# Performance work log

Hardware: AMD Instinct MI355X
Metric: run time of the kernel (lower is better)

## Reference

```python
import jax, jax.numpy as jnp
import numpy as np

BEV_H = 128; BEV_W = 128; HEADS = 8; POINTS = 4; NUM_LAYERS = 6
PC = (-51.2, -51.2, -5.0, 51.2, 51.2, 3.0)
EPS = 1e-5


def _layernorm(x, g, b):
    m = x.mean(-1, keepdims=True)
    v = x.var(-1, keepdims=True)
    return (x - m) * jax.lax.rsqrt(v + 1e-5) * g + b


def _bilinear(feat, loc):
    # feat: (H, W, D); loc: (..., 2) normalized xy in [0, 1]; zero padding outside.
    H, W = feat.shape[0], feat.shape[1]
    ix = loc[..., 0] * W - 0.5
    iy = loc[..., 1] * H - 0.5
    x0 = jnp.floor(ix); y0 = jnp.floor(iy)
    fx = ix - x0; fy = iy - y0
    out = 0.0
    for dx in (0, 1):
        for dy in (0, 1):
            xi = x0 + dx; yi = y0 + dy
            w = (fx if dx else 1.0 - fx) * (fy if dy else 1.0 - fy)
            m = (xi >= 0) & (xi < W) & (yi >= 0) & (yi < H)
            xi_c = jnp.clip(xi, 0, W - 1).astype(jnp.int32)
            yi_c = jnp.clip(yi, 0, H - 1).astype(jnp.int32)
            out = out + (w * m)[..., None] * feat[yi_c, xi_c]
    return out


def _deform_grid(q, value, H, W, ref, ow, ob, aw, ab):
    # Deformable attention over a (H, W) grid of values; q: (Nq, C), value: (H*W, C).
    Nq, C = q.shape
    hd = C // HEADS
    v = value.reshape(H, W, HEADS, hd).transpose(2, 0, 1, 3)            # (h, H, W, hd)
    off = (q @ ow + ob).reshape(Nq, HEADS, POINTS, 2)
    loc = ref[:, None, None, :] + off / jnp.array([W, H], q.dtype)      # (Nq, h, P, 2)
    attn = jax.nn.softmax((q @ aw + ab).reshape(Nq, HEADS, POINTS), axis=-1)
    sampled = jax.vmap(_bilinear)(v, loc.transpose(1, 0, 2, 3))         # (h, Nq, P, hd)
    return jnp.einsum('hnpd,nhp->nhd', sampled, attn).reshape(Nq, C)


def _sca(q, feats, ref_cam, valid, ow, ob, aw, ab):
    # Spatial cross-attention: feats (Ncam, h, Hf, Wf, hd), ref_cam (Ncam, Nq, P, 2),
    # valid (Ncam, Nq, P) float mask of in-frustum projections.
    Nq, C = q.shape
    Hf, Wf = feats.shape[2], feats.shape[3]
    off = (q @ ow + ob).reshape(Nq, HEADS, POINTS, 2)
    loc = ref_cam[:, None] + (off / jnp.array([Wf, Hf], q.dtype)).transpose(1, 0, 2, 3)[None]
    # loc: (Ncam, h, Nq, P, 2)
    attn = jax.nn.softmax((q @ aw + ab).reshape(Nq, HEADS, POINTS), axis=-1)
    sampled = jax.vmap(jax.vmap(_bilinear))(feats, loc)                 # (Ncam, h, Nq, P, hd)
    num = jnp.einsum('chnpd,nhp,cnp->nhd', sampled, attn, valid)
    cnt = jnp.maximum(valid.sum((0, 2)), 1.0)                           # (Nq,)
    return (num / cnt[:, None, None]).reshape(Nq, C)


def _forward(image_feats, camera_intrinsics, camera_extrinsics, prev_bev, bev_embed,
             tsa_vw, tsa_vb, tsa_ow, tsa_ob, tsa_aw, tsa_ab, tsa_pw, tsa_pb,
             sca_vw, sca_vb, sca_ow, sca_ob, sca_aw, sca_ab, sca_pw, sca_pb,
             ffn_w1, ffn_b1, ffn_w2, ffn_b2,
             ln1_g, ln1_b, ln2_g, ln2_b, ln3_g, ln3_b):
    Ncam, C, Hf, Wf = image_feats.shape
    hd = C // HEADS
    Nq = BEV_H * BEV_W
    dt = image_feats.dtype
    feats_flat = image_feats.transpose(0, 2, 3, 1).reshape(Ncam * Hf * Wf, C)

    # 2D reference points for temporal self-attention (each query's own cell).
    xs = (jnp.arange(BEV_W, dtype=dt) + 0.5) / BEV_W
    ys = (jnp.arange(BEV_H, dtype=dt) + 0.5) / BEV_H
    gx, gy = jnp.meshgrid(xs, ys)                                       # (H, W) each
    ref2d = jnp.stack([gx.reshape(-1), gy.reshape(-1)], -1)             # (Nq, 2)

    # 3D pillar reference points projected into each camera.
    xm = PC[0] + gx.reshape(-1) * (PC[3] - PC[0])
    ym = PC[1] + gy.reshape(-1) * (PC[4] - PC[1])
    zm = PC[2] + (jnp.arange(POINTS, dtype=dt) + 0.5) / POINTS * (PC[5] - PC[2])
    ref3d = jnp.stack([
        jnp.broadcast_to(xm[:, None], (Nq, POINTS)),
        jnp.broadcast_to(ym[:, None], (Nq, POINTS)),
        jnp.broadcast_to(zm[None, :], (Nq, POINTS)),
        jnp.ones((Nq, POINTS), dt)], -1)                                # (Nq, P, 4)
    ego2cam = jnp.linalg.inv(camera_extrinsics[0])                      # (Ncam, 4, 4)
    pcam = jnp.einsum('cij,npj->cnpi', ego2cam, ref3d)[..., :3]
    img = jnp.einsum('cij,cnpj->cnpi', camera_intrinsics[0], pcam)
    z = img[..., 2]
    un = img[..., 0] / (jnp.maximum(z, EPS) * Wf)
    vn = img[..., 1] / (jnp.maximum(z, EPS) * Hf)
    valid = ((z > EPS) & (un >= 0) & (un <= 1) & (vn >= 0) & (vn <= 1)).astype(dt)
    ref_cam = jnp.stack([un, vn], -1)                                   # (Ncam, Nq, P, 2)

    q = bev_embed                                                       # (Nq, C)
    prev = prev_bev[:, 0, :]                                            # (Nq, C), B = 1
    for l in range(NUM_LAYERS):
        # Temporal self-attention: deformable sampling from prev BEV + current BEV.
        v_prev = prev @ tsa_vw[l] + tsa_vb[l]
        v_cur = q @ tsa_vw[l] + tsa_vb[l]
        a = 0.5 * (_deform_grid(q, v_prev, BEV_H, BEV_W, ref2d, tsa_ow[l], tsa_ob[l], tsa_aw[l], tsa_ab[l])
                   + _deform_grid(q, v_cur, BEV_H, BEV_W, ref2d, tsa_ow[l], tsa_ob[l], tsa_aw[l], tsa_ab[l]))
        q = _layernorm(q + a @ tsa_pw[l] + tsa_pb[l], ln1_g[l], ln1_b[l])
        # Spatial cross-attention over multi-camera image features.
        v_img = (feats_flat @ sca_vw[l] + sca_vb[l]).reshape(Ncam, Hf, Wf, HEADS, hd).transpose(0, 3, 1, 2, 4)
        a = _sca(q, v_img, ref_cam, valid, sca_ow[l], sca_ob[l], sca_aw[l], sca_ab[l])
        q = _layernorm(q + a @ sca_pw[l] + sca_pb[l], ln2_g[l], ln2_b[l])
        # FFN
        a = jax.nn.relu(q @ ffn_w1[l] + ffn_b1[l]) @ ffn_w2[l] + ffn_b2[l]
        q = _layernorm(q + a, ln3_g[l], ln3_b[l])
    return q.T.reshape(1, C, BEV_H, BEV_W)


def setup_inputs() -> dict:
    key = jax.random.key(0)
    ks = iter(jax.random.split(key, 80))
    def nrm(shape, s=0.02):
        return jax.random.normal(next(ks), shape, jnp.float32) * s
    C, L, Ncam, Hf, Wf = 256, NUM_LAYERS, 6, 58, 100
    Nq = BEV_H * BEV_W
    HP, HP2 = HEADS * POINTS, HEADS * POINTS * 2
    # Structured nuScenes-like cameras: 6 yaws at 60 deg, intrinsics at feature-map scale.
    extr = np.zeros((1, Ncam, 4, 4), np.float32)
    for c in range(Ncam):
        t = c * np.pi / 3.0
        f = np.array([np.cos(t), np.sin(t), 0.0])
        xc = np.array([np.sin(t), -np.cos(t), 0.0])
        yc = np.array([0.0, 0.0, -1.0])
        extr[0, c, :3, :3] = np.stack([xc, yc, f], axis=1)
        extr[0, c, :3, 3] = 1.5 * f + np.array([0.0, 0.0, 1.5])
        extr[0, c, 3, 3] = 1.0
    intr = np.zeros((1, Ncam, 3, 3), np.float32)
    intr[0, :, 0, 0] = 80.0; intr[0, :, 1, 1] = 80.0
    intr[0, :, 0, 2] = Wf / 2.0; intr[0, :, 1, 2] = Hf / 2.0
    intr[0, :, 2, 2] = 1.0
    return {
        'image_feats': jax.random.normal(next(ks), (Ncam, C, Hf, Wf), jnp.float32),
        'camera_intrinsics': jnp.asarray(intr),
        'camera_extrinsics': jnp.asarray(extr),
        'prev_bev': jax.random.normal(next(ks), (Nq, 1, C), jnp.float32),
        'bev_embed': nrm((Nq, C)),
        'tsa_vw': nrm((L, C, C)), 'tsa_vb': jnp.zeros((L, C), jnp.float32),
        'tsa_ow': nrm((L, C, HP2)), 'tsa_ob': nrm((L, HP2), 2.0),
        'tsa_aw': nrm((L, C, HP)), 'tsa_ab': jnp.zeros((L, HP), jnp.float32),
        'tsa_pw': nrm((L, C, C)), 'tsa_pb': jnp.zeros((L, C), jnp.float32),
        'sca_vw': nrm((L, C, C)), 'sca_vb': jnp.zeros((L, C), jnp.float32),
        'sca_ow': nrm((L, C, HP2)), 'sca_ob': nrm((L, HP2), 2.0),
        'sca_aw': nrm((L, C, HP)), 'sca_ab': jnp.zeros((L, HP), jnp.float32),
        'sca_pw': nrm((L, C, C)), 'sca_pb': jnp.zeros((L, C), jnp.float32),
        'ffn_w1': nrm((L, C, 2 * C)), 'ffn_b1': jnp.zeros((L, 2 * C), jnp.float32),
        'ffn_w2': nrm((L, 2 * C, C)), 'ffn_b2': jnp.zeros((L, C), jnp.float32),
        'ln1_g': jnp.ones((L, C), jnp.float32), 'ln1_b': jnp.zeros((L, C), jnp.float32),
        'ln2_g': jnp.ones((L, C), jnp.float32), 'ln2_b': jnp.zeros((L, C), jnp.float32),
        'ln3_g': jnp.ones((L, C), jnp.float32), 'ln3_b': jnp.zeros((L, C), jnp.float32),
    }


def reference(image_feats, camera_intrinsics, camera_extrinsics, prev_bev, bev_embed,
              tsa_vw, tsa_vb, tsa_ow, tsa_ob, tsa_aw, tsa_ab, tsa_pw, tsa_pb,
              sca_vw, sca_vb, sca_ow, sca_ob, sca_aw, sca_ab, sca_pw, sca_pb,
              ffn_w1, ffn_b1, ffn_w2, ffn_b2,
              ln1_g, ln1_b, ln2_g, ln2_b, ln3_g, ln3_b):
    return _forward(image_feats, camera_intrinsics, camera_extrinsics, prev_bev, bev_embed,
                    tsa_vw, tsa_vb, tsa_ow, tsa_ob, tsa_aw, tsa_ab, tsa_pw, tsa_pb,
                    sca_vw, sca_vb, sca_ow, sca_ob, sca_aw, sca_ab, sca_pw, sca_pb,
                    ffn_w1, ffn_b1, ffn_w2, ffn_b2,
                    ln1_g, ln1_b, ln2_g, ln2_b, ln3_g, ln3_b)
```

## Files before the change

### kernel.cpp

```cpp
#include <hip/hip_runtime.h>
#include <hip/hip_bf16.h>
#include <math.h>

typedef __hip_bfloat16 bf16;

#define NQ      16384
#define CDIM    256
#define NHEADS  8
#define NPOINTS 4
#define NCAM    6
#define HF      58
#define WF      100
#define HWF     (HF*WF)
#define NFEAT   (NCAM*HWF)
#define HD      32
#define NLAYERS 6

typedef __attribute__((ext_vector_type(8))) short short8;
typedef __attribute__((ext_vector_type(4))) float floatx4;

__device__ __forceinline__ float toF(float x) { return x; }
__device__ __forceinline__ float toF(bf16 x) { return __bfloat162float(x); }
__device__ __forceinline__ void storeD(float* p, float v) { *p = v; }
__device__ __forceinline__ void storeD(bf16* p, float v) { *p = __float2bfloat16(v); }
// ... 121 lines not shown
                        if (RELU) v = fmaxf(v, 0.f);
                        storeD(&D[(size_t)row * N + col], v);
                    }
                }
            }
        }
    }
}

__global__ __launch_bounds__(256) void gemm_off(
    const bf16* __restrict__ A, const bf16* __restrict__ BT,
    const float* __restrict__ bias, float* __restrict__ D)
{
    __shared__ bf16 As[64 * 32];
    __shared__ bf16 Bs[64 * 32];

    int tid = threadIdx.x;
    int lane = tid & 63, w = tid >> 6;
    int l15 = lane & 15, quad = lane >> 4;
    int bm = blockIdx.y * 64, bn = blockIdx.x * 64;

    floatx4 acc[4];
#pragma unroll
    for (int j = 0; j < 4; j++)
        acc[j] = (floatx4){0.f, 0.f, 0.f, 0.f};

    int rsub = lane >> 2;
    int kc   = (((lane & 3) ^ ((rsub >> 1) & 3))) * 8;
    int sw   = (l15 >> 1) & 3;

    for (int k0 = 0; k0 < 256; k0 += 32) {
        gload_lds16(A + (size_t)(bm + w * 16 + rsub) * 256 + k0 + kc, &As[w * 16 * 32]);
        gload_lds16(BT + (size_t)(bn + w * 16 + rsub) * 256 + k0 + kc, &Bs[w * 16 * 32]);
        __syncthreads();

        short8 a = *(const short8*)(&As[(w * 16 + l15) * 32 + (quad ^ sw) * 8]);
        short8 b[4];
#pragma unroll
        for (int j = 0; j < 4; j++)
            b[j] = *(const short8*)(&Bs[(j * 16 + l15) * 32 + (quad ^ sw) * 8]);
#pragma unroll
        for (int j = 0; j < 4; j++)
            acc[j] = __builtin_amdgcn_mfma_f32_16x16x32_bf16(a, b[j], acc[j], 0, 0, 0);
        __syncthreads();
    }

#pragma unroll
    for (int j = 0; j < 4; j++) {
        int col = bn + j * 16 + l15;
        float bv = bias[col];
#pragma unroll
        for (int r = 0; r < 4; r++) {
            int row = bm + w * 16 + quad * 4 + r;
            D[(size_t)row * 128 + col] = acc[j][r] + bv;
        }
    }
}

__global__ __launch_bounds__(256) void gemm_tsa(
    const bf16* __restrict__ qmean, const bf16* __restrict__ qb,
    const bf16* __restrict__ BT, const float* __restrict__ bias,
    bf16* __restrict__ vgrid, float* __restrict__ offlog)
{
    int bn3 = blockIdx.x;
    int bm = blockIdx.y * 128;
    int bn = bn3 * 128;
    const bf16* A = (bn3 == 2) ? qb : qmean;

    __shared__ bf16 smem[128 * 136];
    bf16* As = smem;
    bf16* Bs = smem + 128 * 32;

    int tid = threadIdx.x;
    int lane = tid & 63, w = tid >> 6;
    int wm = w & 1, wn = w >> 1;
    int l15 = lane & 15, quad = lane >> 4;

    floatx4 acc[4][4];
#pragma unroll
    for (int i = 0; i < 4; i++)
#pragma unroll
        for (int j = 0; j < 4; j++)
            acc[i][j] = (floatx4){0.f, 0.f, 0.f, 0.f};

    int rsub = lane >> 2;
    int kc   = (((lane & 3) ^ ((rsub >> 1) & 3))) * 8;
    int sw   = (l15 >> 1) & 3;

    for (int k0 = 0; k0 < 256; k0 += 32) {
#pragma unroll
        for (int h = 0; h < 2; h++) {
            int r0 = w * 32 + h * 16;
            gload_lds16(A + (size_t)(bm + r0 + rsub) * 256 + k0 + kc, &As[r0 * 32]);
            gload_lds16(BT + (size_t)(bn + r0 + rsub) * 256 + k0 + kc, &Bs[r0 * 32]);
        }
        __syncthreads();

        short8 a[4], b[4];
#pragma unroll
        for (int i = 0; i < 4; i++)
            a[i] = *(const short8*)(&As[(wm * 64 + i * 16 + l15) * 32 + (quad ^ sw) * 8]);
#pragma unroll
        for (int j = 0; j < 4; j++)
            b[j] = *(const short8*)(&Bs[(wn * 64 + j * 16 + l15) * 32 + (quad ^ sw) * 8]);
#pragma unroll
        for (int i = 0; i < 4; i++)
#pragma unroll
            for (int j = 0; j < 4; j++)
                acc[i][j] = __builtin_amdgcn_mfma_f32_16x16x32_bf16(
                    a[i], b[j], acc[i][j], 0, 0, 0);
        __syncthreads();
    }

    if (bn3 < 2) {
#pragma unroll
        for (int i = 0; i < 4; i++) {
#pragma unroll
            for (int j = 0; j < 4; j++) {
                int col = wn * 64 + j * 16 + l15;
                float bv = bias[bn + col];
#pragma unroll
                for (int r = 0; r < 4; r++) {
                    int row = wm * 64 + i * 16 + quad * 4 + r;
                    smem[row * 136 + col] = __float2bfloat16(acc[i][j][r] + bv);
                }
            }
        }
        __syncthreads();
        int lr0 = tid >> 4;
        int ck  = tid & 15;
#pragma unroll
        for (int pass = 0; pass < 8; pass++) {
            int lr = pass * 16 + lr0;
            uint4 v = *(const uint4*)(&smem[lr * 136 + ck * 8]);
            *(uint4*)(vgrid + (size_t)(bm + lr) * 256 + bn + ck * 8) = v;
        }
    } else {
#pragma unroll
        for (int i = 0; i < 4; i++) {
#pragma unroll
            for (int j = 0; j < 4; j++) {
                int col = wn * 64 + j * 16 + l15;
                float bv = bias[256 + col];
#pragma unroll
                for (int r = 0; r < 4; r++) {
                    int row = bm + wm * 64 + i * 16 + quad * 4 + r;
                    offlog[(size_t)row * 128 + col] = acc[i][j][r] + bv;
                }
            }
        }
    }
}

template <bool QM>
__global__ __launch_bounds__(512) void gemm_ln(
    const bf16* __restrict__ A, const bf16* __restrict__ BT,
    const float* __restrict__ bias,
    bf16* __restrict__ qb,
    const float* __restrict__ g, const float* __restrict__ b,
    int K, const bf16* __restrict__ prevb, bf16* __restrict__ qmean)
{
    __shared__ bf16 As[64 * 32];
    __shared__ bf16 Bs[256 * 32];
    __shared__ float red[2][64][4];
    __shared__ float stats[2][64];

    int tid = threadIdx.x;
    int lane = tid & 63, w = tid >> 6;
    int wm = w & 1, wn = w >> 1;
    int l15 = lane & 15, quad = lane >> 4;
    int bm = blockIdx.x * 64;

    floatx4 acc[2][4];
#pragma unroll
    for (int i = 0; i < 2; i++)
#pragma unroll
        for (int j = 0; j < 4; j++)
            acc[i][j] = (floatx4){0.f, 0.f, 0.f, 0.f};

    int rsub = lane >> 2;
    int kc   = (((lane & 3) ^ ((rsub >> 1) & 3))) * 8;
    int sw   = (l15 >> 1) & 3;

    for (int k0 = 0; k0 < K; k0 += 32) {
#pragma unroll
        for (int h = 0; h < 2; h++) {
            int r0 = w * 32 + h * 16;
            gload_lds16(BT + (size_t)(r0 + rsub) * K + k0 + kc, &Bs[r0 * 32]);
        }
        if (w < 4)
            gload_lds16(A + (size_t)(bm + w * 16 + rsub) * K + k0 + kc,
                        &As[w * 16 * 32]);
        __syncthreads();

        short8 a[2], bfr[4];
#pragma unroll
        for (int i = 0; i < 2; i++)
            a[i] = *(const short8*)(&As[(wm * 32 + i * 16 + l15) * 32 + (quad ^ sw) * 8]);
#pragma unroll
        for (int j = 0; j < 4; j++)
            bfr[j] = *(const short8*)(&Bs[(wn * 64 + j * 16 + l15) * 32 + (quad ^ sw) * 8]);
#pragma unroll
        for (int i = 0; i < 2; i++)
#pragma unroll
            for (int j = 0; j < 4; j++)
                acc[i][j] = __builtin_amdgcn_mfma_f32_16x16x32_bf16(
                    a[i], bfr[j], acc[i][j], 0, 0, 0);
        __syncthreads();
    }

    float x[2][4][4];
#pragma unroll
    for (int i = 0; i < 2; i++) {
#pragma unroll
        for (int j = 0; j < 4; j++) {
            int col = wn * 64 + j * 16 + l15;
            float bv = bias[col];
#pragma unroll
            for (int r = 0; r < 4; r++) {
                int row = bm + wm * 32 + i * 16 + quad * 4 + r;
                x[i][j][r] = toF(qb[(size_t)row * CDIM + col]) + acc[i][j][r] + bv;
            }
        }
    }
#pragma unroll
    for (int i = 0; i < 2; i++) {
#pragma unroll
        for (int r = 0; r < 4; r++) {
            float s = x[i][0][r] + x[i][1][r] + x[i][2][r] + x[i][3][r];
            float sq = x[i][0][r] * x[i][0][r] + x[i][1][r] * x[i][1][r] +
                       x[i][2][r] * x[i][2][r] + x[i][3][r] * x[i][3][r];
#pragma unroll
            for (int m = 1; m < 16; m <<= 1) {
                s += __shfl_xor(s, m);
                sq += __shfl_xor(sq, m);
            }
            if (l15 == 0) {
                int rl = wm * 32 + i * 16 + quad * 4 + r;
                red[0][rl][wn] = s;
                red[1][rl][wn] = sq;
            }
        }
    }
    __syncthreads();
    if (tid < 64) {
        float s = red[0][tid][0] + red[0][tid][1] + red[0][tid][2] + red[0][tid][3];
        float sq = red[1][tid][0] + red[1][tid][1] + red[1][tid][2] + red[1][tid][3];
        float mean = s * (1.f / CDIM);
        float var = fmaxf(sq * (1.f / CDIM) - mean * mean, 0.f);
        stats[0][tid] = mean;
        stats[1][tid] = rsqrtf(var + 1e-5f);
    }
    __syncthreads();
#pragma unroll
    for (int i = 0; i < 2; i++) {
#pragma unroll
        for (int j = 0; j < 4; j++) {
            int col = wn * 64 + j * 16 + l15;
            float gc = g[col], bc = b[col];
#pragma unroll
            for (int r = 0; r < 4; r++) {
                int rl = wm * 32 + i * 16 + quad * 4 + r;
                int row = bm + rl;
                float y = (x[i][j][r] - stats[0][rl]) * stats[1][rl] * gc + bc;
                qb[(size_t)row * CDIM + col] = __float2bfloat16(y);
                if (QM)
                    qmean[(size_t)row * CDIM + col] = __float2bfloat16(
                        0.5f * (toF(prevb[(size_t)row * CDIM + col]) + y));
            }
        }
    }
}

template <bool QM>
__global__ __launch_bounds__(512) void ffn_fused(
    const bf16* __restrict__ W1T,
    const float* __restrict__ b1,
    const bf16* __restrict__ W2T,
    const float* __restrict__ b2,
    bf16* __restrict__ qb,
    const float* __restrict__ g, const float* __restrict__ b,
    const bf16* __restrict__ prevb, bf16* __restrict__ qmean)
{
    __shared__ bf16 Hs[64 * 512];
    __shared__ bf16 As[64 * 32];
    __shared__ bf16 Bs[512 * 32];
    __shared__ float red[2][64][4];
    __shared__ float stats[2][64];

    int tid = threadIdx.x;
    int lane = tid & 63, w = tid >> 6;
    int l15 = lane & 15, quad = lane >> 4;
    int bm = blockIdx.x * 64;

    int rsub = lane >> 2;
    int kc   = (((lane & 3) ^ ((rsub >> 1) & 3))) * 8;
    int sw   = (l15 >> 1) & 3;

    {
        floatx4 acc[4][4];
#pragma unroll
        for (int i = 0; i < 4; i++)
#pragma unroll
            for (int j = 0; j < 4; j++)
                acc[i][j] = (floatx4){0.f, 0.f, 0.f, 0.f};

        for (int k0 = 0; k0 < 256; k0 += 32) {
#pragma unroll
            for (int h = 0; h < 4; h++) {
                int r0 = w * 64 + h * 16;
                gload_lds16(W1T + (size_t)(r0 + rsub) * 256 + k0 + kc, &Bs[r0 * 32]);
            }
            if (w < 4)
                gload_lds16(qb + (size_t)(bm + w * 16 + rsub) * 256 + k0 + kc,
                            &As[w * 16 * 32]);
            __syncthreads();

            short8 a[4], bfr[4];
#pragma unroll
            for (int i = 0; i < 4; i++)
                a[i] = *(const short8*)(&As[(i * 16 + l15) * 32 + (quad ^ sw) * 8]);
#pragma unroll
            for (int j = 0; j < 4; j++)
                bfr[j] = *(const short8*)(&Bs[(w * 64 + j * 16 + l15) * 32 + (quad ^ sw) * 8]);
#pragma unroll
            for (int i = 0; i < 4; i++)
#pragma unroll
                for (int j = 0; j < 4; j++)
                    acc[i][j] = __builtin_amdgcn_mfma_f32_16x16x32_bf16(
                        a[i], bfr[j], acc[i][j], 0, 0, 0);
            __syncthreads();
        }

#pragma unroll
        for (int j = 0; j < 4; j++) {
            int col = w * 64 + j * 16 + l15;
            float bv = b1[col];
            int chunk = col >> 3;
            int coff = col & 7;
#pragma unroll
            for (int i = 0; i < 4; i++) {
#pragma unroll
                for (int r = 0; r < 4; r++) {
                    int row = i * 16 + quad * 4 + r;
                    float v = fmaxf(acc[i][j][r] + bv, 0.f);
                    Hs[row * 512 + ((chunk ^ (row & 15)) << 3) + coff] =
                        __float2bfloat16(v);
                }
            }
        }
    }
    __syncthreads();

    int wm = w & 1, wn = w >> 1;

    floatx4 acc[2][4];
#pragma unroll
    for (int i = 0; i < 2; i++)
#pragma unroll
        for (int j = 0; j < 4; j++)
            acc[i][j] = (floatx4){0.f, 0.f, 0.f, 0.f};

    for (int k0 = 0; k0 < 512; k0 += 32) {
#pragma unroll
        for (int h = 0; h < 2; h++) {
            int r0 = w * 32 + h * 16;
            gload_lds16(W2T + (size_t)(r0 + rsub) * 512 + k0 + kc, &Bs[r0 * 32]);
        }
        __syncthreads();

        short8 a[2], bfr[4];
        int kch = (k0 >> 3) + quad;
#pragma unroll
        for (int i = 0; i < 2; i++) {
            int row = wm * 32 + i * 16 + l15;
            a[i] = *(const short8*)(&Hs[row * 512 + ((kch ^ l15) << 3)]);
        }
#pragma unroll
        for (int j = 0; j < 4; j++)
            bfr[j] = *(const short8*)(&Bs[(wn * 64 + j * 16 + l15) * 32 + (quad ^ sw) * 8]);
#pragma unroll
        for (int i = 0; i < 2; i++)
#pragma unroll
            for (int j = 0; j < 4; j++)
                acc[i][j] = __builtin_amdgcn_mfma_f32_16x16x32_bf16(
                    a[i], bfr[j], acc[i][j], 0, 0, 0);
        __syncthreads();
    }

    float x[2][4][4];
#pragma unroll
    for (int i = 0; i < 2; i++) {
#pragma unroll
        for (int j = 0; j < 4; j++) {
            int col = wn * 64 + j * 16 + l15;
            float bv = b2[col];
#pragma unroll
            for (int r = 0; r < 4; r++) {
                int row = bm + wm * 32 + i * 16 + quad * 4 + r;
                x[i][j][r] = toF(qb[(size_t)row * CDIM + col]) + acc[i][j][r] + bv;
            }
        }
    }
#pragma unroll
    for (int i = 0; i < 2; i++) {
#pragma unroll
        for (int r = 0; r < 4; r++) {
            float s = x[i][0][r] + x[i][1][r] + x[i][2][r] + x[i][3][r];
            float sq = x[i][0][r] * x[i][0][r] + x[i][1][r] * x[i][1][r] +
                       x[i][2][r] * x[i][2][r] + x[i][3][r] * x[i][3][r];
#pragma unroll
            for (int m = 1; m < 16; m <<= 1) {
                s += __shfl_xor(s, m);
                sq += __shfl_xor(sq, m);
            }
            if (l15 == 0) {
                int rl = wm * 32 + i * 16 + quad * 4 + r;
                red[0][rl][wn] = s;
                red[1][rl][wn] = sq;
            }
        }
    }
    __syncthreads();
    if (tid < 64) {
// ... 48 lines not shown
{
    __shared__ float tile[32][33];
    int l = blockIdx.z;
    const float* Wl = W + (size_t)l * K * N;
    bf16* WTl = WT + (size_t)l * K * N;
    int k0 = blockIdx.x * 32, n0 = blockIdx.y * 32;
    int tx = threadIdx.x, ty = threadIdx.y;
    for (int i = 0; i < 32; i += 8)
        tile[ty + i][tx] = Wl[(size_t)(k0 + ty + i) * N + n0 + tx];
    __syncthreads();
    for (int i = 0; i < 32; i += 8)
        WTl[(size_t)(n0 + ty + i) * K + k0 + tx] = __float2bfloat16(tile[tx][ty + i]);
}

__global__ void pack_tsa_kernel(const float* __restrict__ vw, const float* __restrict__ vb,
                                const float* __restrict__ ow, const float* __restrict__ ob,
                                const float* __restrict__ aw, const float* __restrict__ ab,
                                bf16* __restrict__ WT, float* __restrict__ BIAS)
{
    int n = blockIdx.x;
    int l = blockIdx.y;
    int k = threadIdx.x;
    float v = 0.f;
    if (n < 256)      v = vw[((size_t)l * 256 + k) * 256 + n];
    else if (n < 320) v = ow[((size_t)l * 256 + k) * 64 + (n - 256)];
    else if (n < 352) v = aw[((size_t)l * 256 + k) * 32 + (n - 320)];
    WT[((size_t)l * 384 + n) * 256 + k] = __float2bfloat16(v);
    if (k == 0) {
        float bv = 0.f;
        if (n < 256)      bv = vb[l * 256 + n];
        else if (n < 320) bv = ob[l * 64 + (n - 256)];
        else if (n < 352) bv = ab[l * 32 + (n - 320)];
        BIAS[l * 384 + n] = bv;
    }
}

__global__ void pack_offattn_kernel(const float* __restrict__ ow, const float* __restrict__ ob,
                                    const float* __restrict__ aw, const float* __restrict__ ab,
                                    bf16* __restrict__ WT, float* __restrict__ BIAS)
{
    int l = blockIdx.y;
    int n = blockIdx.x;
    int k = threadIdx.x;
    float v = 0.f;
    if (n < 64)      v = ow[((size_t)l * 256 + k) * 64 + n];
    else if (n < 96) v = aw[((size_t)l * 256 + k) * 32 + (n - 64)];
    WT[((size_t)l * 128 + n) * 256 + k] = __float2bfloat16(v);
    if (k == 0) {
        float bv = 0.f;
        if (n < 64)      bv = ob[l * 64 + n];
        else if (n < 96) bv = ab[l * 32 + (n - 64)];
        BIAS[l * 128 + n] = bv;
    }
}

__global__ void feats_cvt_kernel(const float* __restrict__ in, bf16* __restrict__ outT)
{
    __shared__ float tile[32][33];
    int c = blockIdx.z;
    int r0 = blockIdx.x * 32, ch0 = blockIdx.y * 32;
    int tx = threadIdx.x, ty = threadIdx.y;
    for (int i = 0; i < 32; i += 8) {
        int r = r0 + tx, ch = ch0 + ty + i;
        tile[ty + i][tx] = (r < HWF) ? in[((size_t)c * CDIM + ch) * HWF + r] : 0.f;
    }
    __syncthreads();
    for (int i = 0; i < 32; i += 8) {
        int r = r0 + ty + i, ch = ch0 + tx;
        if (r < HWF)
            outT[((size_t)c * HWF + r) * CDIM + ch] = __float2bfloat16(tile[tx][ty + i]);
    }
}

__global__ __launch_bounds__(256) void cvt_bf16_kernel(const float* __restrict__ in,
                                                       bf16* __restrict__ out, int n)
{
    int i = blockIdx.x * 256 + threadIdx.x;
    if (i < n) out[i] = __float2bfloat16(in[i]);
}

__global__ void invert4_kernel(const float* __restrict__ extr, float* __restrict__ ego)
{
    int c = threadIdx.x;
    if (c >= NCAM) return;
    float a[4][8];
    for (int i = 0; i < 4; i++)
        for (int j = 0; j < 4; j++) {
            a[i][j] = extr[c * 16 + i * 4 + j];
            a[i][4 + j] = (i == j) ? 1.f : 0.f;
        }
    for (int col = 0; col < 4; col++) {
        int piv = col;
        float best = fabsf(a[col][col]);
        for (int r = col + 1; r < 4; r++) {
            float v = fabsf(a[r][col]);
            if (v > best) { best = v; piv = r; }
        }
        if (piv != col)
            for (int j = 0; j < 8; j++) {
                float t = a[col][j]; a[col][j] = a[piv][j]; a[piv][j] = t;
            }
        float inv = 1.f / a[col][col];
        for (int j = 0; j < 8; j++) a[col][j] *= inv;
        for (int r = 0; r < 4; r++) {
            if (r == col) continue;
            float f = a[r][col];
            for (int j = 0; j < 8; j++) a[r][j] -= f * a[col][j];
        }
    }
    for (int i = 0; i < 4; i++)
        for (int j = 0; j < 4; j++)
            ego[c * 16 + i * 4 + j] = a[i][4 + j];
}

__global__ __launch_bounds__(256) void refcam_compact_kernel(
    const float* __restrict__ ego, const float* __restrict__ intr,
    float4* __restrict__ entries, int* __restrict__ cnt)
{
    int n = blockIdx.x * 256 + threadIdx.x;
    if (n >= NQ) return;

    float gx = ((n & 127) + 0.5f) / 128.0f;
    float gy = ((n >> 7) + 0.5f) / 128.0f;
    float xm = -51.2f + gx * 102.4f;
    float ym = -51.2f + gy * 102.4f;

    float4* out = entries + (size_t)n * 24;
    int k = 0;
    for (int c = 0; c < NCAM; c++) {
        const float* E = ego + c * 16;
        const float* I = intr + c * 9;
#pragma unroll
        for (int p = 0; p < NPOINTS; p++) {
            float zm = -5.0f + (p + 0.5f) * 2.0f;
            float pc[3];
#pragma unroll
            for (int i = 0; i < 3; i++)
                pc[i] = E[i * 4 + 0] * xm + E[i * 4 + 1] * ym + E[i * 4 + 2] * zm + E[i * 4 + 3];
            float im[3];
#pragma unroll
            for (int i = 0; i < 3; i++)
                im[i] = I[i * 3 + 0] * pc[0] + I[i * 3 + 1] * pc[1] + I[i * 3 + 2] * pc[2];
            float z = im[2];
            float zc = fmaxf(z, 1e-5f);
            float un = im[0] / (zc * (float)WF);
            float vn = im[1] / (zc * (float)HF);
            if (z > 1e-5f && un >= 0.f && un <= 1.f && vn >= 0.f && vn <= 1.f) {
                out[k] = make_float4(un, vn, __int_as_float(c * 4 + p), 0.f);
                k++;
            }
        }
    }
    cnt[n] = k;
}

__global__ __launch_bounds__(256) void tsa_sample_kernel(
    const bf16* __restrict__ vgrid, const float* __restrict__ offlog,
    bf16* __restrict__ outA)
{
    int blk = blockIdx.x;
    int qq = (blk & 7) * 512 + (blk >> 3);
    int t = threadIdx.x;
    int n = qq * 4 + (t >> 6);
    int r = t & 63;
    int h = r >> 3;
    int dq = r & 7;
    int col = h * HD + dq * 4;

    const float* fl = offlog + (size_t)n * 128;
    const float* lg = fl + 64 + h * 4;
    float l0 = lg[0], l1 = lg[1], l2 = lg[2], l3 = lg[3];
    float mx = fmaxf(fmaxf(l0, l1), fmaxf(l2, l3));
    float e0 = expf(l0 - mx), e1 = expf(l1 - mx), e2 = expf(l2 - mx), e3 = expf(l3 - mx);
    float inv = 1.f / (e0 + e1 + e2 + e3);
    float w[4] = { e0 * inv, e1 * inv, e2 * inv, e3 * inv };

    const float* of = fl + h * 8;
    float rx = ((n & 127) + 0.5f) / 128.f;
    float ry = ((n >> 7) + 0.5f) / 128.f;

    float a0 = 0.f, a1 = 0.f, a2 = 0.f, a3 = 0.f;
#pragma unroll
    for (int p = 0; p < NPOINTS; p++) {
        float lx = rx + of[p * 2] * (1.f / 128.f);
        float ly = ry + of[p * 2 + 1] * (1.f / 128.f);
        float ix = lx * 128.f - 0.5f;
        float iy = ly * 128.f - 0.5f;
        float xf = floorf(ix), yf = floorf(iy);
        float fx = ix - xf, fy = iy - yf;
        int x0 = (int)xf, y0 = (int)yf;
#pragma unroll
        for (int dy = 0; dy < 2; dy++) {
            int yi = y0 + dy;
            if (yi < 0 || yi >= 128) continue;
            float wy = dy ? fy : 1.f - fy;
#pragma unroll
            for (int dx = 0; dx < 2; dx++) {
                int xi = x0 + dx;
                if (xi < 0 || xi >= 128) continue;
                float wgt = w[p] * wy * (dx ? fx : 1.f - fx);
                uint2 v = *(const uint2*)(vgrid + (size_t)(yi * 128 + xi) * 256 + col);
                a0 += wgt * bfLo(v.x);
                a1 += wgt * bfHi(v.x);
                a2 += wgt * bfLo(v.y);
                a3 += wgt * bfHi(v.y);
            }
        }
    }
    union { bf16 b[4]; uint2 u; } pk;
    pk.b[0] = __float2bfloat16(a0);
    pk.b[1] = __float2bfloat16(a1);
    pk.b[2] = __float2bfloat16(a2);
    pk.b[3] = __float2bfloat16(a3);
    *(uint2*)(outA + (size_t)n * CDIM + col) = pk.u;
}

__global__ __launch_bounds__(256) void sca_sample_kernel(
    const bf16* __restrict__ vimg, const float* __restrict__ offlog,
    const float4* __restrict__ entries, const int* __restrict__ cnt,
    bf16* __restrict__ outA)
{
    int blk = blockIdx.x;
    int qo = (blk & 7) * 256 + (blk >> 3);
    int t = threadIdx.x;
    int n = qo * 8 + (t >> 5);
    int r = t & 31;
    int h = r >> 2;
    int d8 = r & 3;
    int col = h * HD + d8 * 8;

    const float* fl = offlog + (size_t)n * 128;
    const float* lg = fl + 64 + h * 4;
    float l0 = lg[0], l1 = lg[1], l2 = lg[2], l3 = lg[3];
    float mx = fmaxf(fmaxf(l0, l1), fmaxf(l2, l3));
    float e0 = expf(l0 - mx), e1 = expf(l1 - mx), e2 = expf(l2 - mx), e3 = expf(l3 - mx);
    float inv = 1.f / (e0 + e1 + e2 + e3);
    float w[4] = { e0 * inv, e1 * inv, e2 * inv, e3 * inv };

    const float* of = fl + h * 8;
    float ox[4], oy[4];
#pragma unroll
    for (int p = 0; p < NPOINTS; p++) {
        ox[p] = of[p * 2] * (1.f / (float)WF);
        oy[p] = of[p * 2 + 1] * (1.f / (float)HF);
    }

    int ne = cnt[n];
    const float4* ent = entries + (size_t)n * 24;

    float a0 = 0.f, a1 = 0.f, a2 = 0.f, a3 = 0.f;
    float a4 = 0.f, a5 = 0.f, a6 = 0.f, a7 = 0.f;
    for (int e = 0; e < ne; e++) {
        float4 E = ent[e];
        int cp = __float_as_int(E.z);
        int c = cp >> 2, p = cp & 3;
        float lx = E.x + ox[p];
        float ly = E.y + oy[p];
        float ix = lx * (float)WF - 0.5f;
        float iy = ly * (float)HF - 0.5f;
        float xf = floorf(ix), yf = floorf(iy);
        float fx = ix - xf, fy = iy - yf;
        int x0 = (int)xf, y0 = (int)yf;
        float wp_ = w[p];
        const bf16* vb = vimg + (size_t)c * HWF * CDIM;
#pragma unroll
        for (int dy = 0; dy < 2; dy++) {
            int yi = y0 + dy;
            if (yi < 0 || yi >= HF) continue;
            float wy = dy ? fy : 1.f - fy;
#pragma unroll
            for (int dx = 0; dx < 2; dx++) {
                int xi = x0 + dx;
                if (xi < 0 || xi >= WF) continue;
                float wgt = wp_ * wy * (dx ? fx : 1.f - fx);
                uint4 u = *(const uint4*)(vb + (size_t)(yi * WF + xi) * CDIM + col);
                a0 += wgt * bfLo(u.x);
                a1 += wgt * bfHi(u.x);
                a2 += wgt * bfLo(u.y);
                a3 += wgt * bfHi(u.y);
                a4 += wgt * bfLo(u.z);
                a5 += wgt * bfHi(u.z);
                a6 += wgt * bfLo(u.w);
                a7 += wgt * bfHi(u.w);
            }
        }
    }
    float ic = 1.f / fmaxf((float)ne, 1.f);
    union { bf16 b[8]; uint4 u; } pk;
    pk.b[0] = __float2bfloat16(a0 * ic);
    pk.b[1] = __float2bfloat16(a1 * ic);
    pk.b[2] = __float2bfloat16(a2 * ic);
    pk.b[3] = __float2bfloat16(a3 * ic);
    pk.b[4] = __float2bfloat16(a4 * ic);
    pk.b[5] = __float2bfloat16(a5 * ic);
    pk.b[6] = __float2bfloat16(a6 * ic);
    pk.b[7] = __float2bfloat16(a7 * ic);
    *(uint4*)(outA + (size_t)n * CDIM + col) = pk.u;
}

__global__ void out_transpose_kernel(const bf16* __restrict__ qb, float* __restrict__ out)
{
    __shared__ float tile[32][33];
    int n0 = blockIdx.x * 32;
    int c0 = blockIdx.y * 32;
    int tx = threadIdx.x, ty = threadIdx.y;
    for (int i = 0; i < 32; i += 8)
        tile[ty + i][tx] = toF(qb[(size_t)(n0 + ty + i) * CDIM + c0 + tx]);
    __syncthreads();
    for (int i = 0; i < 32; i += 8)
        out[(size_t)(c0 + ty + i) * NQ + n0 + tx] = tile[tx][ty + i];
}

extern "C" void kernel_launch(void* const* d_in, const int* in_sizes, int n_in,
                              void* d_out, int out_size, void* d_ws, size_t ws_size,
                              hipStream_t stream)
{
    const float* image_feats = (const float*)d_in[0];
    const float* intr        = (const float*)d_in[1];
    const float* extr        = (const float*)d_in[2];
    const float* prev_bev    = (const float*)d_in[3];
    const float* bev_embed   = (const float*)d_in[4];
    const float* tsa_vw = (const float*)d_in[5];
    const float* tsa_vb = (const float*)d_in[6];
    const float* tsa_ow = (const float*)d_in[7];
    const float* tsa_ob = (const float*)d_in[8];
    const float* tsa_aw = (const float*)d_in[9];
    const float* tsa_ab = (const float*)d_in[10];
    const float* tsa_pw = (const float*)d_in[11];
    const float* tsa_pb = (const float*)d_in[12];
    const float* sca_vw = (const float*)d_in[13];
    const float* sca_vb = (const float*)d_in[14];
    const float* sca_ow = (const float*)d_in[15];
    const float* sca_ob = (const float*)d_in[16];
    const float* sca_aw = (const float*)d_in[17];
    const float* sca_ab = (const float*)d_in[18];
    const float* sca_pw = (const float*)d_in[19];
    const float* sca_pb = (const float*)d_in[20];
    const float* ffn_w1 = (const float*)d_in[21];
    const float* ffn_b1 = (const float*)d_in[22];
    const float* ffn_w2 = (const float*)d_in[23];
    const float* ffn_b2 = (const float*)d_in[24];
    const float* ln1_g  = (const float*)d_in[25];
    const float* ln1_b  = (const float*)d_in[26];
    const float* ln2_g  = (const float*)d_in[27];
    const float* ln2_b  = (const float*)d_in[28];
    const float* ln3_g  = (const float*)d_in[29];
    const float* ln3_b  = (const float*)d_in[30];

    char* wp = (char*)d_ws;
    auto alloc = [&](size_t bytes) -> void* {
        void* r = (void*)wp;
        wp += (bytes + 255) & ~(size_t)255;
        return r;
    };
    bf16*  prevbf = (bf16*) alloc((size_t)NQ * CDIM * 2);
    bf16*  qb     = (bf16*) alloc((size_t)NQ * CDIM * 2);
    bf16*  qmeanb = (bf16*) alloc((size_t)NQ * CDIM * 2);
    bf16*  attnA  = (bf16*) alloc((size_t)NQ * CDIM * 2);
    float* offlog = (float*)alloc((size_t)NQ * 128 * 4);
    float4* entries = (float4*)alloc((size_t)NQ * 24 * 16);
    int*   entcnt = (int*)  alloc((size_t)NQ * 4);
    float* ego    = (float*)alloc(128 * 4);
    bf16*  featsT = (bf16*) alloc((size_t)NFEAT * CDIM * 2);
    bf16*  pwT  = (bf16*)alloc((size_t)NLAYERS * 65536 * 2);
    bf16*  svwT = (bf16*)alloc((size_t)NLAYERS * 65536 * 2);
    bf16*  spwT = (bf16*)alloc((size_t)NLAYERS * 65536 * 2);
    bf16*  w1T  = (bf16*)alloc((size_t)NLAYERS * 131072 * 2);
    bf16*  w2T  = (bf16*)alloc((size_t)NLAYERS * 131072 * 2);
    bf16*  ptwT = (bf16*)alloc((size_t)NLAYERS * 384 * 256 * 2);
    float* ptb  = (float*)alloc((size_t)NLAYERS * 384 * 4);
    bf16*  sowT = (bf16*)alloc((size_t)NLAYERS * 32768 * 2);
    float* sobF = (float*)alloc((size_t)NLAYERS * 128 * 4);
    bf16*  vgrid = (bf16*)alloc((size_t)NQ * CDIM * 2);
    bf16*  vimg6 = (bf16*)alloc((size_t)NLAYERS * NFEAT * CDIM * 2);

    dim3 blk32(32, 8);

    cvt_bf16_kernel<<<(NQ * CDIM + 255) / 256, 256, 0, stream>>>(bev_embed, qb, NQ * CDIM);
    cvt_bf16_kernel<<<(NQ * CDIM + 255) / 256, 256, 0, stream>>>(prev_bev, prevbf, NQ * CDIM);
    qmean_kernel<<<NQ * CDIM / 8 / 256, 256, 0, stream>>>(prevbf, qb, qmeanb);
    invert4_kernel<<<1, 64, 0, stream>>>(extr, ego);
    refcam_compact_kernel<<<NQ / 256, 256, 0, stream>>>(ego, intr, entries, entcnt);
    {
        dim3 g((HWF + 31) / 32, CDIM / 32, NCAM);
        feats_cvt_kernel<<<g, blk32, 0, stream>>>(image_feats, featsT);
    }
    wt_cvt_kernel<<<dim3(8, 8,  NLAYERS), blk32, 0, stream>>>(tsa_pw, pwT,  256, 256);
    wt_cvt_kernel<<<dim3(8, 8,  NLAYERS), blk32, 0, stream>>>(sca_vw, svwT, 256, 256);
    wt_cvt_kernel<<<dim3(8, 8,  NLAYERS), blk32, 0, stream>>>(sca_pw, spwT, 256, 256);
    wt_cvt_kernel<<<dim3(8, 16, NLAYERS), blk32, 0, stream>>>(ffn_w1, w1T, 256, 512);
    wt_cvt_kernel<<<dim3(16, 8, NLAYERS), blk32, 0, stream>>>(ffn_w2, w2T, 512, 256);
    pack_tsa_kernel<<<dim3(384, NLAYERS), 256, 0, stream>>>(
        tsa_vw, tsa_vb, tsa_ow, tsa_ob, tsa_aw, tsa_ab, ptwT, ptb);
    pack_offattn_kernel<<<dim3(128, NLAYERS), 256, 0, stream>>>(
        sca_ow, sca_ob, sca_aw, sca_ab, sowT, sobF);
    gemm_mfma<bf16, false, true, true><<<dim3(2 * NLAYERS * 272), 256, 0, stream>>>(
        featsT, svwT, sca_vb, vimg6, NFEAT, CDIM, CDIM,
        65536, 256, (size_t)NFEAT * CDIM);

    for (int l = 0; l < NLAYERS; l++) {
        gemm_tsa<<<dim3(3, NQ / 128), 256, 0, stream>>>(
            qmeanb, qb, ptwT + (size_t)l * 98304, ptb + l * 384, vgrid, offlog);
        tsa_sample_kernel<<<NQ / 4, 256, 0, stream>>>(vgrid, offlog, attnA);
        gemm_ln<false><<<NQ / 64, 512, 0, stream>>>(
            attnA, pwT + (size_t)l * 65536, tsa_pb + l * CDIM,
            qb, ln1_g + l * CDIM, ln1_b + l * CDIM, CDIM, nullptr, nullptr);

        gemm_off<<<dim3(2, NQ / 64), 256, 0, stream>>>(
            qb, sowT + (size_t)l * 32768, sobF + l * 128, offlog);
        sca_sample_kernel<<<NQ / 8, 256, 0, stream>>>(
            vimg6 + (size_t)l * NFEAT * CDIM, offlog, entries, entcnt, attnA);
        gemm_ln<false><<<NQ / 64, 512, 0, stream>>>(
            attnA, spwT + (size_t)l * 65536, sca_pb + l * CDIM,
            qb, ln2_g + l * CDIM, ln2_b + l * CDIM, CDIM, nullptr, nullptr);

        if (l < NLAYERS - 1)
            ffn_fused<true><<<NQ / 64, 512, 0, stream>>>(
                w1T + (size_t)l * 131072, ffn_b1 + l * 512,
                w2T + (size_t)l * 131072, ffn_b2 + l * CDIM,
                qb, ln3_g + l * CDIM, ln3_b + l * CDIM, prevbf, qmeanb);
        else
            ffn_fused<false><<<NQ / 64, 512, 0, stream>>>(
                w1T + (size_t)l * 131072, ffn_b1 + l * 512,
                w2T + (size_t)l * 131072, ffn_b2 + l * CDIM,
                qb, ln3_g + l * CDIM, ln3_b + l * CDIM, nullptr, nullptr);
    }

    {
        dim3 g(NQ / 32, CDIM / 32);
        out_transpose_kernel<<<g, blk32, 0, stream>>>(qb, (float*)d_out);
    }
}
```

Baseline: 897.3 us.

## Fuse deformable sampling into output-projection+LayerNorm kernels via LDS staging

The separate TSA and SCA sampling kernels are merged into the following projection+residual+LayerNorm GEMM. Each 512-thread block samples its 64 queries straight into a padded LDS A-tile, then runs the shared projection/LN body. This removes the attnA global round-trip and two launches per layer. In exchange, sampling now runs with 256 blocks of 512 threads and large LDS use, so there is less parallelism to hide gather latency, and the earlier block-index swizzle for locality is gone.

```diff
diff --git a/kernel.cpp b/kernel.cpp
--- a/kernel.cpp
+++ b/kernel.cpp
@@ -297,51 +297,42 @@
     }
 }
 
-template <bool QM>
-__global__ __launch_bounds__(512) void gemm_ln(
-    const bf16* __restrict__ A, const bf16* __restrict__ BT,
-    const float* __restrict__ bias,
+__device__ __forceinline__ void proj_ln_body(
+    const bf16* At,
+    bf16* Bs,
+    float (*red)[64][4], float (*stats)[64],
+    const bf16* __restrict__ BT, const float* __restrict__ bias,
     bf16* __restrict__ qb,
     const float* __restrict__ g, const float* __restrict__ b,
-    int K, const bf16* __restrict__ prevb, bf16* __restrict__ qmean)
-{
-    __shared__ bf16 As[64 * 32];
-    __shared__ bf16 Bs[256 * 32];
-    __shared__ float red[2][64][4];
-    __shared__ float stats[2][64];
-
-    int tid = threadIdx.x;
+    int bm, int tid)
+{
     int lane = tid & 63, w = tid >> 6;
     int wm = w & 1, wn = w >> 1;
     int l15 = lane & 15, quad = lane >> 4;
-    int bm = blockIdx.x * 64;
-
-    floatx4 acc[2][4];
-#pragma unroll
-    for (int i = 0; i < 2; i++)
-#pragma unroll
-        for (int j = 0; j < 4; j++)
-            acc[i][j] = (floatx4){0.f, 0.f, 0.f, 0.f};
 
     int rsub = lane >> 2;
     int kc   = (((lane & 3) ^ ((rsub >> 1) & 3))) * 8;
     int sw   = (l15 >> 1) & 3;
 
-    for (int k0 = 0; k0 < K; k0 += 32) {
+    floatx4 acc[2][4];
+#pragma unroll
+    for (int i = 0; i < 2; i++)
+#pragma unroll
+        for (int j = 0; j < 4; j++)
+            acc[i][j] = (floatx4){0.f, 0.f, 0.f, 0.f};
+
+    for (int k0 = 0; k0 < 256; k0 += 32) {
 #pragma unroll
         for (int h = 0; h < 2; h++) {
             int r0 = w * 32 + h * 16;
-            gload_lds16(BT + (size_t)(r0 + rsub) * K + k0 + kc, &Bs[r0 * 32]);
-        }
-        if (w < 4)
-            gload_lds16(A + (size_t)(bm + w * 16 + rsub) * K + k0 + kc,
-                        &As[w * 16 * 32]);
+            gload_lds16(BT + (size_t)(r0 + rsub) * 256 + k0 + kc, &Bs[r0 * 32]);
+        }
         __syncthreads();
 
         short8 a[2], bfr[4];
 #pragma unroll
         for (int i = 0; i < 2; i++)
-            a[i] = *(const short8*)(&As[(wm * 32 + i * 16 + l15) * 32 + (quad ^ sw) * 8]);
+            a[i] = *(const short8*)(&At[(wm * 32 + i * 16 + l15) * 264 + k0 + quad * 8]);
 #pragma unroll
         for (int j = 0; j < 4; j++)
             bfr[j] = *(const short8*)(&Bs[(wn * 64 + j * 16 + l15) * 32 + (quad ^ sw) * 8]);
@@ -409,12 +400,187 @@
                 int row = bm + rl;
                 float y = (x[i][j][r] - stats[0][rl]) * stats[1][rl] * gc + bc;
                 qb[(size_t)row * CDIM + col] = __float2bfloat16(y);
-                if (QM)
-                    qmean[(size_t)row * CDIM + col] = __float2bfloat16(
-                        0.5f * (toF(prevb[(size_t)row * CDIM + col]) + y));
-            }
-        }
-    }
+            }
+        }
+    }
+}
+
+__global__ __launch_bounds__(512) void tsa_fused(
+    const bf16* __restrict__ vgrid, const float* __restrict__ offlog,
+    const bf16* __restrict__ BT, const float* __restrict__ bias,
+    bf16* __restrict__ qb,
+    const float* __restrict__ g, const float* __restrict__ b)
+{
+    __shared__ bf16 At[64 * 264];
+    __shared__ bf16 Bs[256 * 32];
+    __shared__ float red[2][64][4];
+    __shared__ float stats[2][64];
+
+    int tid = threadIdx.x;
+    int bm = blockIdx.x * 64;
+
+    {
+        int qloc = tid >> 6;
+        int r = tid & 63;
+        int h = r >> 3;
+        int dq = r & 7;
+        int col = h * HD + dq * 4;
+#pragma unroll 1
+        for (int pass = 0; pass < 8; pass++) {
+            int nloc = pass * 8 + qloc;
+            int n = bm + nloc;
+            const float* fl = offlog + (size_t)n * 128;
+            const float* lg = fl + 64 + h * 4;
+            float l0 = lg[0], l1 = lg[1], l2 = lg[2], l3 = lg[3];
+            float mx = fmaxf(fmaxf(l0, l1), fmaxf(l2, l3));
+            float e0 = expf(l0 - mx), e1 = expf(l1 - mx);
+            float e2 = expf(l2 - mx), e3 = expf(l3 - mx);
+            float inv = 1.f / (e0 + e1 + e2 + e3);
+            float wgt4[4] = { e0 * inv, e1 * inv, e2 * inv, e3 * inv };
+
+            const float* of = fl + h * 8;
+            float rx = ((n & 127) + 0.5f) / 128.f;
+            float ry = ((n >> 7) + 0.5f) / 128.f;
+
+            float a0 = 0.f, a1 = 0.f, a2 = 0.f, a3 = 0.f;
+#pragma unroll
+            for (int p = 0; p < NPOINTS; p++) {
+                float lx = rx + of[p * 2] * (1.f / 128.f);
+                float ly = ry + of[p * 2 + 1] * (1.f / 128.f);
+                float ix = lx * 128.f - 0.5f;
+                float iy = ly * 128.f - 0.5f;
+                float xf = floorf(ix), yf = floorf(iy);
+                float fx = ix - xf, fy = iy - yf;
+                int x0 = (int)xf, y0 = (int)yf;
+#pragma unroll
+                for (int dy = 0; dy < 2; dy++) {
+                    int yi = y0 + dy;
+                    if (yi < 0 || yi >= 128) continue;
+                    float wy = dy ? fy : 1.f - fy;
+#pragma unroll
+                    for (int dx = 0; dx < 2; dx++) {
+                        int xi = x0 + dx;
+                        if (xi < 0 || xi >= 128) continue;
+                        float wgt = wgt4[p] * wy * (dx ? fx : 1.f - fx);
+                        uint2 v = *(const uint2*)(vgrid + (size_t)(yi * 128 + xi) * 256 + col);
+                        a0 += wgt * bfLo(v.x);
+                        a1 += wgt * bfHi(v.x);
+                        a2 += wgt * bfLo(v.y);
+                        a3 += wgt * bfHi(v.y);
+                    }
+                }
+            }
+            union { bf16 bb[4]; uint2 u; } pk;
+            pk.bb[0] = __float2bfloat16(a0);
+            pk.bb[1] = __float2bfloat16(a1);
+            pk.bb[2] = __float2bfloat16(a2);
+            pk.bb[3] = __float2bfloat16(a3);
+            *(uint2*)(&At[nloc * 264 + col]) = pk.u;
+        }
+    }
+    __syncthreads();
+
+    proj_ln_body(At, Bs, red, stats, BT, bias, qb, g, b, bm, tid);
+}
+
+__global__ __launch_bounds__(512) void sca_fused(
+    const bf16* __restrict__ vimg, const float* __restrict__ offlog,
+    const float4* __restrict__ entries, const int* __restrict__ cnt,
+    const bf16* __restrict__ BT, const float* __restrict__ bias,
+    bf16* __restrict__ qb,
+    const float* __restrict__ g, const float* __restrict__ b)
+{
+    __shared__ bf16 At[64 * 264];
+    __shared__ bf16 Bs[256 * 32];
+    __shared__ float red[2][64][4];
+    __shared__ float stats[2][64];
+
+    int tid = threadIdx.x;
+    int bm = blockIdx.x * 64;
+
+    {
+        int qloc = tid >> 5;
+        int r = tid & 31;
+        int h = r >> 2;
+        int d8 = r & 3;
+        int col = h * HD + d8 * 8;
+#pragma unroll 1
+        for (int pass = 0; pass < 4; pass++) {
+            int nloc = pass * 16 + qloc;
+            int n = bm + nloc;
+            const float* fl = offlog + (size_t)n * 128;
+            const float* lg = fl + 64 + h * 4;
+            float l0 = lg[0], l1 = lg[1], l2 = lg[2], l3 = lg[3];
+            float mx = fmaxf(fmaxf(l0, l1), fmaxf(l2, l3));
+            float e0 = expf(l0 - mx), e1 = expf(l1 - mx);
+            float e2 = expf(l2 - mx), e3 = expf(l3 - mx);
+            float inv = 1.f / (e0 + e1 + e2 + e3);
+            float wgt4[4] = { e0 * inv, e1 * inv, e2 * inv, e3 * inv };
+
+            const float* of = fl + h * 8;
+            float ox[4], oy[4];
+#pragma unroll
+            for (int p = 0; p < NPOINTS; p++) {
+                ox[p] = of[p * 2] * (1.f / (float)WF);
+                oy[p] = of[p * 2 + 1] * (1.f / (float)HF);
+            }
+
+            int ne = cnt[n];
+            const float4* ent = entries + (size_t)n * 24;
+
+            float a0 = 0.f, a1 = 0.f, a2 = 0.f, a3 = 0.f;
+            float a4 = 0.f, a5 = 0.f, a6 = 0.f, a7 = 0.f;
+            for (int e = 0; e < ne; e++) {
+                float4 E = ent[e];
+                int cp = __float_as_int(E.z);
+                int c = cp >> 2, p = cp & 3;
+                float lx = E.x + ox[p];
+                float ly = E.y + oy[p];
+                float ix = lx * (float)WF - 0.5f;
+                float iy = ly * (float)HF - 0.5f;
+                float xf = floorf(ix), yf = floorf(iy);
+                float fx = ix - xf, fy = iy - yf;
+                int x0 = (int)xf, y0 = (int)yf;
+                float wp_ = wgt4[p];
+                const bf16* vb = vimg + (size_t)c * HWF * CDIM;
+#pragma unroll
+                for (int dy = 0; dy < 2; dy++) {
+                    int yi = y0 + dy;
+                    if (yi < 0 || yi >= HF) continue;
+                    float wy = dy ? fy : 1.f - fy;
+#pragma unroll
+                    for (int dx = 0; dx < 2; dx++) {
+                        int xi = x0 + dx;
+                        if (xi < 0 || xi >= WF) continue;
+                        float wgt = wp_ * wy * (dx ? fx : 1.f - fx);
+                        uint4 u = *(const uint4*)(vb + (size_t)(yi * WF + xi) * CDIM + col);
+                        a0 += wgt * bfLo(u.x);
+                        a1 += wgt * bfHi(u.x);
+                        a2 += wgt * bfLo(u.y);
+                        a3 += wgt * bfHi(u.y);
+                        a4 += wgt * bfLo(u.z);
+                        a5 += wgt * bfHi(u.z);
+                        a6 += wgt * bfLo(u.w);
+                        a7 += wgt * bfHi(u.w);
+                    }
+                }
+            }
+            float ic = 1.f / fmaxf((float)ne, 1.f);
+            union { bf16 bb[8]; uint4 u; } pk;
+            pk.bb[0] = __float2bfloat16(a0 * ic);
+            pk.bb[1] = __float2bfloat16(a1 * ic);
+            pk.bb[2] = __float2bfloat16(a2 * ic);
+            pk.bb[3] = __float2bfloat16(a3 * ic);
+            pk.bb[4] = __float2bfloat16(a4 * ic);
+            pk.bb[5] = __float2bfloat16(a5 * ic);
+            pk.bb[6] = __float2bfloat16(a6 * ic);
+            pk.bb[7] = __float2bfloat16(a7 * ic);
+            *(uint4*)(&At[nloc * 264 + col]) = pk.u;
+        }
+    }
+    __syncthreads();
+
+    proj_ln_body(At, Bs, red, stats, BT, bias, qb, g, b, bm, tid);
 }
 
 template <bool QM>
@@ -769,150 +935,6 @@
         }
     }
     cnt[n] = k;
-}
-
-__global__ __launch_bounds__(256) void tsa_sample_kernel(
-    const bf16* __restrict__ vgrid, const float* __restrict__ offlog,
-    bf16* __restrict__ outA)
-{
-    int blk = blockIdx.x;
-    int qq = (blk & 7) * 512 + (blk >> 3);
-    int t = threadIdx.x;
-    int n = qq * 4 + (t >> 6);
-    int r = t & 63;
-    int h = r >> 3;
-    int dq = r & 7;
-    int col = h * HD + dq * 4;
-
-    const float* fl = offlog + (size_t)n * 128;
-    const float* lg = fl + 64 + h * 4;
-    float l0 = lg[0], l1 = lg[1], l2 = lg[2], l3 = lg[3];
-    float mx = fmaxf(fmaxf(l0, l1), fmaxf(l2, l3));
-    float e0 = expf(l0 - mx), e1 = expf(l1 - mx), e2 = expf(l2 - mx), e3 = expf(l3 - mx);
-    float inv = 1.f / (e0 + e1 + e2 + e3);
-    float w[4] = { e0 * inv, e1 * inv, e2 * inv, e3 * inv };
-
-    const float* of = fl + h * 8;
-    float rx = ((n & 127) + 0.5f) / 128.f;
-    float ry = ((n >> 7) + 0.5f) / 128.f;
-
-    float a0 = 0.f, a1 = 0.f, a2 = 0.f, a3 = 0.f;
-#pragma unroll
-    for (int p = 0; p < NPOINTS; p++) {
-        float lx = rx + of[p * 2] * (1.f / 128.f);
-        float ly = ry + of[p * 2 + 1] * (1.f / 128.f);
-        float ix = lx * 128.f - 0.5f;
-        float iy = ly * 128.f - 0.5f;
-        float xf = floorf(ix), yf = floorf(iy);
-        float fx = ix - xf, fy = iy - yf;
-        int x0 = (int)xf, y0 = (int)yf;
-#pragma unroll
-        for (int dy = 0; dy < 2; dy++) {
-            int yi = y0 + dy;
-            if (yi < 0 || yi >= 128) continue;
-            float wy = dy ? fy : 1.f - fy;
-#pragma unroll
-            for (int dx = 0; dx < 2; dx++) {
-                int xi = x0 + dx;
-                if (xi < 0 || xi >= 128) continue;
-                float wgt = w[p] * wy * (dx ? fx : 1.f - fx);
-                uint2 v = *(const uint2*)(vgrid + (size_t)(yi * 128 + xi) * 256 + col);
-                a0 += wgt * bfLo(v.x);
-                a1 += wgt * bfHi(v.x);
-                a2 += wgt * bfLo(v.y);
-                a3 += wgt * bfHi(v.y);
-            }
-        }
-    }
-    union { bf16 b[4]; uint2 u; } pk;
-    pk.b[0] = __float2bfloat16(a0);
-    pk.b[1] = __float2bfloat16(a1);
-    pk.b[2] = __float2bfloat16(a2);
-    pk.b[3] = __float2bfloat16(a3);
-    *(uint2*)(outA + (size_t)n * CDIM + col) = pk.u;
-}
-
-__global__ __launch_bounds__(256) void sca_sample_kernel(
-    const bf16* __restrict__ vimg, const float* __restrict__ offlog,
-    const float4* __restrict__ entries, const int* __restrict__ cnt,
-    bf16* __restrict__ outA)
-{
-    int blk = blockIdx.x;
-    int qo = (blk & 7) * 256 + (blk >> 3);
-    int t = threadIdx.x;
-    int n = qo * 8 + (t >> 5);
-    int r = t & 31;
-    int h = r >> 2;
-    int d8 = r & 3;
-    int col = h * HD + d8 * 8;
-
-    const float* fl = offlog + (size_t)n * 128;
-    const float* lg = fl + 64 + h * 4;
-    float l0 = lg[0], l1 = lg[1], l2 = lg[2], l3 = lg[3];
-    float mx = fmaxf(fmaxf(l0, l1), fmaxf(l2, l3));
-    float e0 = expf(l0 - mx), e1 = expf(l1 - mx), e2 = expf(l2 - mx), e3 = expf(l3 - mx);
-    float inv = 1.f / (e0 + e1 + e2 + e3);
-    float w[4] = { e0 * inv, e1 * inv, e2 * inv, e3 * inv };
-
-    const float* of = fl + h * 8;
-    float ox[4], oy[4];
-#pragma unroll
-    for (int p = 0; p < NPOINTS; p++) {
-        ox[p] = of[p * 2] * (1.f / (float)WF);
-        oy[p] = of[p * 2 + 1] * (1.f / (float)HF);
-    }
-
-    int ne = cnt[n];
-    const float4* ent = entries + (size_t)n * 24;
-
-    float a0 = 0.f, a1 = 0.f, a2 = 0.f, a3 = 0.f;
-    float a4 = 0.f, a5 = 0.f, a6 = 0.f, a7 = 0.f;
-    for (int e = 0; e < ne; e++) {
-        float4 E = ent[e];
-        int cp = __float_as_int(E.z);
-        int c = cp >> 2, p = cp & 3;
-        float lx = E.x + ox[p];
-        float ly = E.y + oy[p];
-        float ix = lx * (float)WF - 0.5f;
-        float iy = ly * (float)HF - 0.5f;
-        float xf = floorf(ix), yf = floorf(iy);
-        float fx = ix - xf, fy = iy - yf;
-        int x0 = (int)xf, y0 = (int)yf;
-        float wp_ = w[p];
-        const bf16* vb = vimg + (size_t)c * HWF * CDIM;
-#pragma unroll
-        for (int dy = 0; dy < 2; dy++) {
-            int yi = y0 + dy;
-            if (yi < 0 || yi >= HF) continue;
-            float wy = dy ? fy : 1.f - fy;
-#pragma unroll
-            for (int dx = 0; dx < 2; dx++) {
-                int xi = x0 + dx;
-                if (xi < 0 || xi >= WF) continue;
-                float wgt = wp_ * wy * (dx ? fx : 1.f - fx);
-                uint4 u = *(const uint4*)(vb + (size_t)(yi * WF + xi) * CDIM + col);
-                a0 += wgt * bfLo(u.x);
-                a1 += wgt * bfHi(u.x);
-                a2 += wgt * bfLo(u.y);
-                a3 += wgt * bfHi(u.y);
-                a4 += wgt * bfLo(u.z);
-                a5 += wgt * bfHi(u.z);
-                a6 += wgt * bfLo(u.w);
-                a7 += wgt * bfHi(u.w);
-            }
-        }
-    }
-    float ic = 1.f / fmaxf((float)ne, 1.f);
-    union { bf16 b[8]; uint4 u; } pk;
-    pk.b[0] = __float2bfloat16(a0 * ic);
-    pk.b[1] = __float2bfloat16(a1 * ic);
-    pk.b[2] = __float2bfloat16(a2 * ic);
-    pk.b[3] = __float2bfloat16(a3 * ic);
-    pk.b[4] = __float2bfloat16(a4 * ic);
-    pk.b[5] = __float2bfloat16(a5 * ic);
-    pk.b[6] = __float2bfloat16(a6 * ic);
-    pk.b[7] = __float2bfloat16(a7 * ic);
-    *(uint4*)(outA + (size_t)n * CDIM + col) = pk.u;
 }
 
 __global__ void out_transpose_kernel(const bf16* __restrict__ qb, float* __restrict__ out)
@@ -973,7 +995,6 @@
     bf16*  prevbf = (bf16*) alloc((size_t)NQ * CDIM * 2);
     bf16*  qb     = (bf16*) alloc((size_t)NQ * CDIM * 2);
     bf16*  qmeanb = (bf16*) alloc((size_t)NQ * CDIM * 2);
-    bf16*  attnA  = (bf16*) alloc((size_t)NQ * CDIM * 2);
     float* offlog = (float*)alloc((size_t)NQ * 128 * 4);
     float4* entries = (float4*)alloc((size_t)NQ * 24 * 16);
     int*   entcnt = (int*)  alloc((size_t)NQ * 4);
@@ -1018,18 +1039,16 @@
     for (int l = 0; l < NLAYERS; l++) {
         gemm_tsa<<<dim3(3, NQ / 128), 256, 0, stream>>>(
             qmeanb, qb, ptwT + (size_t)l * 98304, ptb + l * 384, vgrid, offlog);
-        tsa_sample_kernel<<<NQ / 4, 256, 0, stream>>>(vgrid, offlog, attnA);
-        gemm_ln<false><<<NQ / 64, 512, 0, stream>>>(
-            attnA, pwT + (size_t)l * 65536, tsa_pb + l * CDIM,
-            qb, ln1_g + l * CDIM, ln1_b + l * CDIM, CDIM, nullptr, nullptr);
+        tsa_fused<<<NQ / 64, 512, 0, stream>>>(
+            vgrid, offlog, pwT + (size_t)l * 65536, tsa_pb + l * CDIM,
+            qb, ln1_g + l * CDIM, ln1_b + l * CDIM);
 
         gemm_off<<<dim3(2, NQ / 64), 256, 0, stream>>>(
             qb, sowT + (size_t)l * 32768, sobF + l * 128, offlog);
-        sca_sample_kernel<<<NQ / 8, 256, 0, stream>>>(
-            vimg6 + (size_t)l * NFEAT * CDIM, offlog, entries, entcnt, attnA);
-        gemm_ln<false><<<NQ / 64, 512, 0, stream>>>(
-            attnA, spwT + (size_t)l * 65536, sca_pb + l * CDIM,
-            qb, ln2_g + l * CDIM, ln2_b + l * CDIM, CDIM, nullptr, nullptr);
+        sca_fused<<<NQ / 64, 512, 0, stream>>>(
+            vimg6 + (size_t)l * NFEAT * CDIM, offlog, entries, entcnt,
+            spwT + (size_t)l * 65536, sca_pb + l * CDIM,
+            qb, ln2_g + l * CDIM, ln2_b + l * CDIM);
 
         if (l < NLAYERS - 1)
             ffn_fused<true><<<NQ / 64, 512, 0, stream>>>(
```

Result: slower. 1.140 ms (+27.1%).
